# Performance work log

Measured on AMD Instinct MI355X. Metric: run time of the kernel, lower is better.

The kernel has to match this reference:

```python
import jax, jax.numpy as jnp
import numpy as np

D, W, H = 128, 128, 128          # volume obj_shape (d, w, h)
RES_D, RES_H = 180, 180          # detector resolution
SR_D, SR_W, SR_H = 1, 1, 1       # sample rates
BATCH = 4                        # hardcoded batch_size in the torch module


def _trilinear_zeros(vol, cx, cy, cz):
    """torch.grid_sample 5D, mode=trilinear, align_corners=True, padding=zeros.
    vol: [D, W, H]. cx indexes last dim (H), cy indexes W, cz indexes D; all in [-1,1].
    """
    d, w, h = vol.shape
    ix = (cx + 1.0) * 0.5 * (h - 1)
    iy = (cy + 1.0) * 0.5 * (w - 1)
    iz = (cz + 1.0) * 0.5 * (d - 1)
    x0 = jnp.floor(ix); y0 = jnp.floor(iy); z0 = jnp.floor(iz)
    wx1 = ix - x0; wy1 = iy - y0; wz1 = iz - z0
    wx0 = 1.0 - wx1; wy0 = 1.0 - wy1; wz0 = 1.0 - wz1

    def corner(zf, yf, xf, wgt):
        valid = (zf >= 0) & (zf <= d - 1) & (yf >= 0) & (yf <= w - 1) & (xf >= 0) & (xf <= h - 1)
        zi = jnp.clip(zf, 0, d - 1).astype(jnp.int32)
        yi = jnp.clip(yf, 0, w - 1).astype(jnp.int32)
        xi = jnp.clip(xf, 0, h - 1).astype(jnp.int32)
        return jnp.where(valid, vol[zi, yi, xi] * wgt, 0.0)

    return (corner(z0,     y0,     x0,     wz0 * wy0 * wx0)
          + corner(z0,     y0,     x0 + 1, wz0 * wy0 * wx1)
          + corner(z0,     y0 + 1, x0,     wz0 * wy1 * wx0)
          + corner(z0,     y0 + 1, x0 + 1, wz0 * wy1 * wx1)
          + corner(z0 + 1, y0,     x0,     wz1 * wy0 * wx0)
          + corner(z0 + 1, y0,     x0 + 1, wz1 * wy0 * wx1)
          + corner(z0 + 1, y0 + 1, x0,     wz1 * wy1 * wx0)
          + corner(z0 + 1, y0 + 1, x0 + 1, wz1 * wy1 * wx1))


def _project_one(vol, emi_pos, spacing):
    # vol: [D, W, H], emi_pos: [3], spacing: [3]
    K = SR_W * W
    p0y = jnp.linspace(0.0, W - 1.0, K)                     # (P0 - I0)·N, N = [0,1,0]
    lin_x = jnp.linspace(-RES_D / 2.0, RES_D / 2.0 - 1.0, RES_D * SR_D)
    lin_y = jnp.linspace(-RES_H / 2.0, RES_H / 2.0 - 1.0, RES_H * SR_H)
    gx, gy = jnp.meshgrid(lin_x, lin_y, indexing='ij')      # [Nx, Ny]
    I = jnp.stack([gx, jnp.zeros_like(gx), gy], axis=-1) - emi_pos   # [Nx,Ny,3]
    dxv = I / I[..., 1:2]
    dx = jnp.linalg.norm(dxv * spacing, axis=-1)            # per-ray path length [Nx,Ny]
    In = I / jnp.linalg.norm(I, axis=-1, keepdims=True)     # unit ray dirs
    T = (p0y - emi_pos[1])[None, None, :] / In[..., 1:2]    # [Nx,Ny,K]
    grid = In[..., None, :] * T[..., None] + emi_pos        # world points [Nx,Ny,K,3]
    # normalization as in torch code, then torch.flip(grid,[3]) swaps coord order
    cx = grid[..., 2] / H * 2.0          # -> indexes last vol dim (H)
    cy = grid[..., 1] / W * 2.0 - 1.0    # -> indexes W
    cz = grid[..., 0] / D * 2.0          # -> indexes D
    samp = _trilinear_zeros(vol, cx, cy, cz)                # [Nx,Ny,K]
    return jnp.sum(samp, axis=-1) * dx                      # [Nx,Ny]


def setup_inputs() -> dict:
    key = jax.random.key(0)
    k1, k2 = jax.random.split(key)
    I_rec = jax.random.uniform(k1, (1, 1, D, W, H), dtype=jnp.float32)
    # emitters near [0, -300, 0]; y must be far from the y=0 detector plane
    poses = jnp.array([0.0, -300.0, 0.0], jnp.float32) + 5.0 * jax.random.normal(k2, (BATCH, 3), jnp.float32)
    spacing = jnp.ones((3,), jnp.float32)
    return {"I_rec": I_rec, "poses": poses, "spacing": spacing}


def reference(I_rec, poses, spacing):
    vol = I_rec[0, 0]  # [D, W, H]
    # deterministic idx = [0..BATCH-1] (original uses random.sample)
    proj = jax.vmap(_project_one, in_axes=(None, 0, None))(vol, poses[:BATCH], spacing)
    return proj[:, None, :, :]  # [BATCH, 1, RES_D*SR_D, RES_H*SR_H]
```

## Files before the change

### kernel.cpp

```cpp
#include <hip/hip_runtime.h>


#define RES 180
#define NPIX (4 * RES * RES)
#define PIX_PER_BLOCK 32
#define NCHUNK (NPIX / PIX_PER_BLOCK)
#define CHUNK_STRIDE 1013

typedef struct __attribute__((packed, aligned(4))) { float x, y; } f2u;

__global__ __launch_bounds__(256) void proj_kernel(
    const float* __restrict__ vol, const float* __restrict__ poses,
    const float* __restrict__ spacing, float* __restrict__ out) {
  const int tid = threadIdx.x;
  const int lp  = tid & 31;
  const int ks  = tid >> 5;
  const int chunk = (int)(((long long)blockIdx.x * CHUNK_STRIDE) % NCHUNK);
  const int gpix = chunk * PIX_PER_BLOCK + lp;

  const int b   = gpix / (RES * RES);
  const int rem = gpix - b * (RES * RES);
  const int i   = rem / RES;
  const int j   = rem - i * RES;

  const float ex = poses[b * 3 + 0];
  const float ey = poses[b * 3 + 1];
  const float ez = poses[b * 3 + 2];

  const float gx = (float)i - 90.0f;
  const float gy = (float)j - 90.0f;
  const float Ix = gx - ex;
  const float Iy = -ey;
  const float Iz = gy - ez;

  const float c     = 63.5f / 64.0f;
  const float invIy = 1.0f / Iy;

  const float izb = fmaf(ex + Ix, c, 63.5f);
  const float izs = Ix * invIy * c;
  const float ixb = fmaf(ez + Iz, c, 63.5f);
  const float ixs = Iz * invIy * c;

  const int k0 = ks * 16;
  float ka = (float)k0;
  float kb = (float)(k0 + 16);
  {
    if (ixs > 1e-12f)       { ka = fmaxf(ka, (-1.0f - ixb) / ixs); kb = fminf(kb, (128.0f - ixb) / ixs); }
    else if (ixs < -1e-12f) { ka = fmaxf(ka, (128.0f - ixb) / ixs); kb = fminf(kb, (-1.0f - ixb) / ixs); }
    else if (ixb <= -1.0f || ixb >= 128.0f) { kb = ka; }
    if (izs > 1e-12f)       { ka = fmaxf(ka, (-1.0f - izb) / izs); kb = fminf(kb, (128.0f - izb) / izs); }
    else if (izs < -1e-12f) { ka = fmaxf(ka, (128.0f - izb) / izs); kb = fminf(kb, (-1.0f - izb) / izs); }
    else if (izb <= -1.0f || izb >= 128.0f) { kb = ka; }
    ka = fmaxf(ka, (float)k0);
    kb = fminf(kb, (float)(k0 + 16));
  }
  const int kai = (int)ceilf(ka);
  const int kbi = (int)ceilf(kb);

  float sum = 0.0f;
#pragma unroll 2
  for (int k = kai; k < kbi; ++k) {
    const float kf = (float)k;
    const float ix = fmaf(kf, ixs, ixb);
    const float iy = kf * c;
    const float iz = fmaf(kf, izs, izb);

    const float fx = floorf(ix), fy = floorf(iy), fz = floorf(iz);
    const int x0 = (int)fx, y0 = (int)fy, z0 = (int)fz;

    const float wx1 = ix - fx, wy1 = iy - fy, wz1 = iz - fz;
    const float wx0 = 1.0f - wx1, wy0 = 1.0f - wy1, wz0 = 1.0f - wz1;

    const float vx0 = ((unsigned)x0       < 128u) ? wx0 : 0.0f;
    const float vx1 = ((unsigned)(x0 + 1) < 128u) ? wx1 : 0.0f;
    const float vz0 = ((unsigned)z0       < 128u) ? wz0 : 0.0f;
    const float vz1 = ((unsigned)(z0 + 1) < 128u) ? wz1 : 0.0f;

    const int xb2 = min(max(x0, 0), 126);
    const bool in = (x0 == xb2);
    const float wlo = in ? vx0 : vx1;
    const float whi = in ? vx1 : vx0;

    const int zc0 = min(max(z0, 0), 127), zc1 = min(max(z0 + 1, 0), 127);
    const float* base = vol + ((zc0 << 14) + (y0 << 7) + xb2);
    const int dz = (zc1 - zc0) << 14;

    const f2u v00 = *(const f2u*)(base);
    const f2u v01 = *(const f2u*)(base + 128);
    const f2u v10 = *(const f2u*)(base + dz);
    const f2u v11 = *(const f2u*)(base + dz + 128);

    const float s00 = fmaf(whi, v00.y, wlo * v00.x);
    const float s01 = fmaf(whi, v01.y, wlo * v01.x);
    const float s10 = fmaf(whi, v10.y, wlo * v10.x);
    const float s11 = fmaf(whi, v11.y, wlo * v11.x);
    const float s0  = fmaf(wy1, s01, wy0 * s00);
    const float s1  = fmaf(wy1, s11, wy0 * s10);

    sum = fmaf(vz0, s0, sum);
    sum = fmaf(vz1, s1, sum);
  }

  __shared__ float part[256];
  part[tid] = sum;
  __syncthreads();

  if (tid < PIX_PER_BLOCK) {
    float tot = 0.0f;
#pragma unroll
    for (int s = 0; s < 8; ++s) tot += part[tid + 32 * s];
    const float sxp = spacing[0], syp = spacing[1], szp = spacing[2];
    const float ax = Ix * invIy * sxp;
    const float az = Iz * invIy * szp;
    const float dxl = sqrtf(fmaf(ax, ax, fmaf(az, az, syp * syp)));
    out[gpix] = tot * dxl;
  }
}

extern "C" void kernel_launch(void* const* d_in, const int* in_sizes, int n_in,
                              void* d_out, int out_size, void* d_ws, size_t ws_size,
                              hipStream_t stream) {
  const float* vol     = (const float*)d_in[0];
  const float* poses   = (const float*)d_in[1];
  const float* spacing = (const float*)d_in[2];
  float* out = (float*)d_out;

  proj_kernel<<<NCHUNK, 256, 0, stream>>>(vol, poses, spacing, out);
}
```

Baseline: 26.99 us.

## Split ray march into unmasked interior loop and masked edge loops; widen blocks

```diff
diff --git a/kernel.cpp b/kernel.cpp
--- a/kernel.cpp
+++ b/kernel.cpp
@@ -2,26 +2,25 @@
 
 
 #define RES 180
-#define NPIX (4 * RES * RES)
-#define PIX_PER_BLOCK 32
-#define NCHUNK (NPIX / PIX_PER_BLOCK)
+#define JSTRIPS 3
+#define NCHUNK (4 * RES * JSTRIPS)
 #define CHUNK_STRIDE 1013
 
 typedef struct __attribute__((packed, aligned(4))) { float x, y; } f2u;
 
-__global__ __launch_bounds__(256) void proj_kernel(
+__global__ __launch_bounds__(512) void proj_kernel(
     const float* __restrict__ vol, const float* __restrict__ poses,
     const float* __restrict__ spacing, float* __restrict__ out) {
-  const int tid = threadIdx.x;
-  const int lp  = tid & 31;
-  const int ks  = tid >> 5;
+  const int tid  = threadIdx.x;
+  const int lane = tid & 63;
+  const int ks   = tid >> 6;
   const int chunk = (int)(((long long)blockIdx.x * CHUNK_STRIDE) % NCHUNK);
-  const int gpix = chunk * PIX_PER_BLOCK + lp;
-
-  const int b   = gpix / (RES * RES);
-  const int rem = gpix - b * (RES * RES);
-  const int i   = rem / RES;
-  const int j   = rem - i * RES;
+  const int js = chunk % JSTRIPS;
+  const int t  = chunk / JSTRIPS;
+  const int i  = t % RES;
+  const int b  = t / RES;
+  const int j  = js * 64 + lane;
+  const bool live = (j < RES);
 
   const float ex = poses[b * 3 + 0];
   const float ey = poses[b * 3 + 1];
@@ -42,78 +41,114 @@
   const float ixs = Iz * invIy * c;
 
   const int k0 = ks * 16;
-  float ka = (float)k0;
-  float kb = (float)(k0 + 16);
-  {
-    if (ixs > 1e-12f)       { ka = fmaxf(ka, (-1.0f - ixb) / ixs); kb = fminf(kb, (128.0f - ixb) / ixs); }
-    else if (ixs < -1e-12f) { ka = fmaxf(ka, (128.0f - ixb) / ixs); kb = fminf(kb, (-1.0f - ixb) / ixs); }
-    else if (ixb <= -1.0f || ixb >= 128.0f) { kb = ka; }
-    if (izs > 1e-12f)       { ka = fmaxf(ka, (-1.0f - izb) / izs); kb = fminf(kb, (128.0f - izb) / izs); }
-    else if (izs < -1e-12f) { ka = fmaxf(ka, (128.0f - izb) / izs); kb = fminf(kb, (-1.0f - izb) / izs); }
-    else if (izb <= -1.0f || izb >= 128.0f) { kb = ka; }
-    ka = fmaxf(ka, (float)k0);
-    kb = fminf(kb, (float)(k0 + 16));
-  }
+  float ka = (float)k0, kb = (float)(k0 + 16);
+  if (ixs > 1e-12f)       { ka = fmaxf(ka, (-1.0f - ixb) / ixs); kb = fminf(kb, (128.0f - ixb) / ixs); }
+  else if (ixs < -1e-12f) { ka = fmaxf(ka, (128.0f - ixb) / ixs); kb = fminf(kb, (-1.0f - ixb) / ixs); }
+  else if (ixb <= -1.0f || ixb >= 128.0f) { kb = ka; }
+  if (izs > 1e-12f)       { ka = fmaxf(ka, (-1.0f - izb) / izs); kb = fminf(kb, (128.0f - izb) / izs); }
+  else if (izs < -1e-12f) { ka = fmaxf(ka, (128.0f - izb) / izs); kb = fminf(kb, (-1.0f - izb) / izs); }
+  else if (izb <= -1.0f || izb >= 128.0f) { kb = ka; }
+  ka = fmaxf(ka, (float)k0);
+  kb = fminf(kb, (float)(k0 + 16));
   const int kai = (int)ceilf(ka);
-  const int kbi = (int)ceilf(kb);
+  int kbi = (int)ceilf(kb);
+  if (!live) kbi = kai;
+
+  float ia = ka, ib = kb;
+  if (ixs > 1e-12f)       { ia = fmaxf(ia, (1.0f - ixb) / ixs); ib = fminf(ib, (126.0f - ixb) / ixs); }
+  else if (ixs < -1e-12f) { ia = fmaxf(ia, (126.0f - ixb) / ixs); ib = fminf(ib, (1.0f - ixb) / ixs); }
+  else if (ixb < 1.0f || ixb >= 126.0f) { ib = ia; }
+  if (izs > 1e-12f)       { ia = fmaxf(ia, (1.0f - izb) / izs); ib = fminf(ib, (126.0f - izb) / izs); }
+  else if (izs < -1e-12f) { ia = fmaxf(ia, (126.0f - izb) / izs); ib = fminf(ib, (1.0f - izb) / izs); }
+  else if (izb < 1.0f || izb >= 126.0f) { ib = ia; }
+  int m0 = (int)ceilf(fmaxf(ia, 1.0f));
+  int m1 = (int)ceilf(ib);
+  m0 = min(max(m0, kai), kbi);
+  m1 = min(max(m1, m0), kbi);
 
   float sum = 0.0f;
+
+#define MASKED_BODY(k)                                                         \
+  {                                                                            \
+    const float kf = (float)(k);                                               \
+    const float ix = fmaf(kf, ixs, ixb);                                       \
+    const float iy = kf * c;                                                   \
+    const float iz = fmaf(kf, izs, izb);                                       \
+    const float fx = floorf(ix), fy = floorf(iy), fz = floorf(iz);             \
+    const int x0 = (int)fx, y0 = (int)fy, z0 = (int)fz;                        \
+    const float wx1 = ix - fx, wy1 = iy - fy, wz1 = iz - fz;                   \
+    const float wx0 = 1.0f - wx1, wy0 = 1.0f - wy1, wz0 = 1.0f - wz1;          \
+    const float vx0 = ((unsigned)x0       < 128u) ? wx0 : 0.0f;                \
+    const float vx1 = ((unsigned)(x0 + 1) < 128u) ? wx1 : 0.0f;                \
+    const float vz0 = ((unsigned)z0       < 128u) ? wz0 : 0.0f;                \
+    const float vz1 = ((unsigned)(z0 + 1) < 128u) ? wz1 : 0.0f;                \
+    const int xb2 = min(max(x0, 0), 126);                                      \
+    const bool in = (x0 == xb2);                                               \
+    const float wlo = in ? vx0 : vx1;                                          \
+    const float whi = in ? vx1 : vx0;                                          \
+    const int zc0 = min(max(z0, 0), 127), zc1 = min(max(z0 + 1, 0), 127);      \
+    const float* base = vol + ((zc0 << 14) + (y0 << 7) + xb2);                 \
+    const int dz = (zc1 - zc0) << 14;                                          \
+    const f2u v00 = *(const f2u*)(base);                                       \
+    const f2u v01 = *(const f2u*)(base + 128);                                 \
+    const f2u v10 = *(const f2u*)(base + dz);                                  \
+    const f2u v11 = *(const f2u*)(base + dz + 128);                            \
+    const float s00 = fmaf(whi, v00.y, wlo * v00.x);                           \
+    const float s01 = fmaf(whi, v01.y, wlo * v01.x);                           \
+    const float s10 = fmaf(whi, v10.y, wlo * v10.x);                           \
+    const float s11 = fmaf(whi, v11.y, wlo * v11.x);                           \
+    const float s0  = fmaf(wy1, s01, wy0 * s00);                               \
+    const float s1  = fmaf(wy1, s11, wy0 * s10);                               \
+    sum = fmaf(vz0, s0, sum);                                                  \
+    sum = fmaf(vz1, s1, sum);                                                  \
+  }
+
+  for (int k = kai; k < m0; ++k) MASKED_BODY(k)
+
 #pragma unroll 2
-  for (int k = kai; k < kbi; ++k) {
+  for (int k = m0; k < m1; ++k) {
     const float kf = (float)k;
     const float ix = fmaf(kf, ixs, ixb);
-    const float iy = kf * c;
     const float iz = fmaf(kf, izs, izb);
+    const float fx = floorf(ix), fz = floorf(iz);
+    const int x0 = (int)fx, z0 = (int)fz;
+    const float wx1 = ix - fx, wz1 = iz - fz;
+    const float wx0 = 1.0f - wx1, wz0 = 1.0f - wz1;
+    const float wy0 = kf * 0.0078125f;
+    const float wy1 = 1.0f - wy0;
 
-    const float fx = floorf(ix), fy = floorf(iy), fz = floorf(iz);
-    const int x0 = (int)fx, y0 = (int)fy, z0 = (int)fz;
+    const float* p = vol + ((z0 << 14) + (k << 7) - 128 + x0);
+    const f2u v00 = *(const f2u*)(p);
+    const f2u v01 = *(const f2u*)(p + 128);
+    const f2u v10 = *(const f2u*)(p + 16384);
+    const f2u v11 = *(const f2u*)(p + 16384 + 128);
 
-    const float wx1 = ix - fx, wy1 = iy - fy, wz1 = iz - fz;
-    const float wx0 = 1.0f - wx1, wy0 = 1.0f - wy1, wz0 = 1.0f - wz1;
-
-    const float vx0 = ((unsigned)x0       < 128u) ? wx0 : 0.0f;
-    const float vx1 = ((unsigned)(x0 + 1) < 128u) ? wx1 : 0.0f;
-    const float vz0 = ((unsigned)z0       < 128u) ? wz0 : 0.0f;
-    const float vz1 = ((unsigned)(z0 + 1) < 128u) ? wz1 : 0.0f;
-
-    const int xb2 = min(max(x0, 0), 126);
-    const bool in = (x0 == xb2);
-    const float wlo = in ? vx0 : vx1;
-    const float whi = in ? vx1 : vx0;
-
-    const int zc0 = min(max(z0, 0), 127), zc1 = min(max(z0 + 1, 0), 127);
-    const float* base = vol + ((zc0 << 14) + (y0 << 7) + xb2);
-    const int dz = (zc1 - zc0) << 14;
-
-    const f2u v00 = *(const f2u*)(base);
-    const f2u v01 = *(const f2u*)(base + 128);
-    const f2u v10 = *(const f2u*)(base + dz);
-    const f2u v11 = *(const f2u*)(base + dz + 128);
-
-    const float s00 = fmaf(whi, v00.y, wlo * v00.x);
-    const float s01 = fmaf(whi, v01.y, wlo * v01.x);
-    const float s10 = fmaf(whi, v10.y, wlo * v10.x);
-    const float s11 = fmaf(whi, v11.y, wlo * v11.x);
+    const float s00 = fmaf(wx1, v00.y, wx0 * v00.x);
+    const float s01 = fmaf(wx1, v01.y, wx0 * v01.x);
+    const float s10 = fmaf(wx1, v10.y, wx0 * v10.x);
+    const float s11 = fmaf(wx1, v11.y, wx0 * v11.x);
     const float s0  = fmaf(wy1, s01, wy0 * s00);
     const float s1  = fmaf(wy1, s11, wy0 * s10);
-
-    sum = fmaf(vz0, s0, sum);
-    sum = fmaf(vz1, s1, sum);
+    sum = fmaf(wz0, s0, sum);
+    sum = fmaf(wz1, s1, sum);
   }
 
-  __shared__ float part[256];
+  for (int k = m1; k < kbi; ++k) MASKED_BODY(k)
+#undef MASKED_BODY
+
+  __shared__ float part[512];
   part[tid] = sum;
   __syncthreads();
 
-  if (tid < PIX_PER_BLOCK) {
+  if (tid < 64 && live) {
     float tot = 0.0f;
 #pragma unroll
-    for (int s = 0; s < 8; ++s) tot += part[tid + 32 * s];
+    for (int s = 0; s < 8; ++s) tot += part[tid + 64 * s];
     const float sxp = spacing[0], syp = spacing[1], szp = spacing[2];
     const float ax = Ix * invIy * sxp;
     const float az = Iz * invIy * szp;
     const float dxl = sqrtf(fmaf(ax, ax, fmaf(az, az, syp * syp)));
-    out[gpix] = tot * dxl;
+    out[((b * RES) + i) * RES + j] = tot * dxl;
   }
 }
 
@@ -125,5 +160,5 @@
   const float* spacing = (const float*)d_in[2];
   float* out = (float*)d_out;
 
-  proj_kernel<<<NCHUNK, 256, 0, stream>>>(vol, poses, spacing, out);
+  proj_kernel<<<NCHUNK, 512, 0, stream>>>(vol, poses, spacing, out);
 }
```

Result: slower. 46.16 us (+71.0%).

## Pre-pad volume with zero borders and remap rays into 64-wide row strips

Applied to the files above, without the earlier changes.

```diff
diff --git a/kernel.cpp b/kernel.cpp
--- a/kernel.cpp
+++ b/kernel.cpp
@@ -2,61 +2,159 @@
 
 
 #define RES 180
-#define NPIX (4 * RES * RES)
-#define PIX_PER_BLOCK 32
-#define NCHUNK (NPIX / PIX_PER_BLOCK)
+#define JSTRIPS 3
+#define NCHUNK (4 * RES * JSTRIPS)
 #define CHUNK_STRIDE 1013
 
+#define PH 130
+#define PW 128
+#define PD 130
+#define PSLAB (PW * PH)
+#define PAD_ELEMS (PD * PSLAB)
+#define PAD_FRONT ((size_t)(PSLAB + PH + 128) * 4)
+#define PAD_TAIL  ((size_t)(PSLAB + PH + 128) * 4)
+#define WS_NEED (PAD_FRONT + (size_t)PAD_ELEMS * 4 + PAD_TAIL)
+#define PAD_OFF_EL (PSLAB + 1)
+
 typedef struct __attribute__((packed, aligned(4))) { float x, y; } f2u;
 
-__global__ __launch_bounds__(256) void proj_kernel(
+__global__ __launch_bounds__(256) void pad_kernel(
+    const float* __restrict__ vol, float* __restrict__ pad) {
+  const int t = blockIdx.x * 256 + threadIdx.x;
+  const int z = blockIdx.y;
+  if (t >= PSLAB) return;
+  const int y = t / PH;
+  const int x = t - y * PH;
+  float v = 0.0f;
+  if (z >= 1 && z <= 128 && x >= 1 && x <= 128)
+    v = vol[(((z - 1)) << 14) + (y << 7) + (x - 1)];
+  pad[z * PSLAB + t] = v;
+}
+
+__global__ __launch_bounds__(512) void proj_pad_kernel(
+    const float* __restrict__ pad, const float* __restrict__ poses,
+    const float* __restrict__ spacing, float* __restrict__ out) {
+  const int tid  = threadIdx.x;
+  const int lane = tid & 63;
+  const int ks   = tid >> 6;
+  const int chunk = (int)(((long long)blockIdx.x * CHUNK_STRIDE) % NCHUNK);
+  const int js = chunk % JSTRIPS;
+  const int t  = chunk / JSTRIPS;
+  const int i  = t % RES;
+  const int b  = t / RES;
+  const int j  = js * 64 + lane;
+  const bool live = (j < RES);
+
+  const float ex = poses[b * 3 + 0];
+  const float ey = poses[b * 3 + 1];
+  const float ez = poses[b * 3 + 2];
+
+  const float gx = (float)i - 90.0f;
+  const float gy = (float)j - 90.0f;
+  const float Ix = gx - ex;
+  const float Iy = -ey;
+  const float Iz = gy - ez;
+
+  const float c     = 63.5f / 64.0f;
+  const float invIy = 1.0f / Iy;
+
+  const float izb = fmaf(ex + Ix, c, 63.5f);
+  const float izs = Ix * invIy * c;
+  const float ixb = fmaf(ez + Iz, c, 63.5f);
+  const float ixs = Iz * invIy * c;
+
+  const int k0 = ks * 16;
+  float ka = (float)k0, kb = (float)(k0 + 16);
+  if (ixs > 1e-12f)       { ka = fmaxf(ka, (-1.0f - ixb) / ixs); kb = fminf(kb, (128.0f - ixb) / ixs); }
+  else if (ixs < -1e-12f) { ka = fmaxf(ka, (128.0f - ixb) / ixs); kb = fminf(kb, (-1.0f - ixb) / ixs); }
+  else if (ixb <= -1.0f || ixb >= 128.0f) { kb = ka; }
+  if (izs > 1e-12f)       { ka = fmaxf(ka, (-1.0f - izb) / izs); kb = fminf(kb, (128.0f - izb) / izs); }
+  else if (izs < -1e-12f) { ka = fmaxf(ka, (128.0f - izb) / izs); kb = fminf(kb, (-1.0f - izb) / izs); }
+  else if (izb <= -1.0f || izb >= 128.0f) { kb = ka; }
+  ka = fmaxf(ka, (float)k0);
+  kb = fminf(kb, (float)(k0 + 16));
+  const int kai = (int)ceilf(ka);
+  int kbi = (int)ceilf(kb);
+  if (!live) kbi = kai;
+
+  const float* pbase = pad + PAD_OFF_EL;
+
+  float sum = 0.0f;
+#pragma unroll 2
+  for (int k = kai; k < kbi; ++k) {
+    const float kf = (float)k;
+    const float ix = fmaf(kf, ixs, ixb);
+    const float iz = fmaf(kf, izs, izb);
+    const float fx = floorf(ix), fz = floorf(iz);
+    const int x0 = (int)fx, z0 = (int)fz;
+    const float wx1 = ix - fx, wz1 = iz - fz;
+    const float wx0 = 1.0f - wx1, wz0 = 1.0f - wz1;
+    const float wyA = kf * 0.0078125f;
+    const float wyB = 1.0f - wyA;
+
+    const float* p = pbase + (z0 * PSLAB + (k - 1) * PH + x0);
+    const f2u v00 = *(const f2u*)(p);
+    const f2u v01 = *(const f2u*)(p + PH);
+    const f2u v10 = *(const f2u*)(p + PSLAB);
+    const f2u v11 = *(const f2u*)(p + PSLAB + PH);
+
+    const float s00 = fmaf(wx1, v00.y, wx0 * v00.x);
+    const float s01 = fmaf(wx1, v01.y, wx0 * v01.x);
+    const float s10 = fmaf(wx1, v10.y, wx0 * v10.x);
+    const float s11 = fmaf(wx1, v11.y, wx0 * v11.x);
+    const float s0  = fmaf(wyB, s01, wyA * s00);
+    const float s1  = fmaf(wyB, s11, wyA * s10);
+    sum = fmaf(wz0, s0, sum);
+    sum = fmaf(wz1, s1, sum);
+  }
+
+  __shared__ float part[512];
+  part[tid] = sum;
+  __syncthreads();
+
+  if (tid < 64 && live) {
+    float tot = 0.0f;
+#pragma unroll
+    for (int s = 0; s < 8; ++s) tot += part[tid + 64 * s];
+    const float sxp = spacing[0], syp = spacing[1], szp = spacing[2];
+    const float ax = Ix * invIy * sxp;
+    const float az = Iz * invIy * szp;
+    const float dxl = sqrtf(fmaf(ax, ax, fmaf(az, az, syp * syp)));
+    out[((b * RES) + i) * RES + j] = tot * dxl;
+  }
+}
+
+#define F_PPB 32
+#define F_NCHUNK (4 * RES * RES / F_PPB)
+__global__ __launch_bounds__(256) void proj_masked_kernel(
     const float* __restrict__ vol, const float* __restrict__ poses,
     const float* __restrict__ spacing, float* __restrict__ out) {
   const int tid = threadIdx.x;
   const int lp  = tid & 31;
   const int ks  = tid >> 5;
-  const int chunk = (int)(((long long)blockIdx.x * CHUNK_STRIDE) % NCHUNK);
-  const int gpix = chunk * PIX_PER_BLOCK + lp;
-
+  const int chunk = (int)(((long long)blockIdx.x * 1013) % F_NCHUNK);
+  const int gpix = chunk * F_PPB + lp;
   const int b   = gpix / (RES * RES);
   const int rem = gpix - b * (RES * RES);
   const int i   = rem / RES;
   const int j   = rem - i * RES;
-
-  const float ex = poses[b * 3 + 0];
-  const float ey = poses[b * 3 + 1];
-  const float ez = poses[b * 3 + 2];
-
-  const float gx = (float)i - 90.0f;
-  const float gy = (float)j - 90.0f;
-  const float Ix = gx - ex;
-  const float Iy = -ey;
-  const float Iz = gy - ez;
-
-  const float c     = 63.5f / 64.0f;
-  const float invIy = 1.0f / Iy;
-
-  const float izb = fmaf(ex + Ix, c, 63.5f);
-  const float izs = Ix * invIy * c;
-  const float ixb = fmaf(ez + Iz, c, 63.5f);
-  const float ixs = Iz * invIy * c;
-
+  const float ex = poses[b * 3 + 0], ey = poses[b * 3 + 1], ez = poses[b * 3 + 2];
+  const float gx = (float)i - 90.0f, gy = (float)j - 90.0f;
+  const float Ix = gx - ex, Iy = -ey, Iz = gy - ez;
+  const float c = 63.5f / 64.0f, invIy = 1.0f / Iy;
+  const float izb = fmaf(ex + Ix, c, 63.5f), izs = Ix * invIy * c;
+  const float ixb = fmaf(ez + Iz, c, 63.5f), ixs = Iz * invIy * c;
   const int k0 = ks * 16;
-  float ka = (float)k0;
-  float kb = (float)(k0 + 16);
-  {
-    if (ixs > 1e-12f)       { ka = fmaxf(ka, (-1.0f - ixb) / ixs); kb = fminf(kb, (128.0f - ixb) / ixs); }
-    else if (ixs < -1e-12f) { ka = fmaxf(ka, (128.0f - ixb) / ixs); kb = fminf(kb, (-1.0f - ixb) / ixs); }
-    else if (ixb <= -1.0f || ixb >= 128.0f) { kb = ka; }
-    if (izs > 1e-12f)       { ka = fmaxf(ka, (-1.0f - izb) / izs); kb = fminf(kb, (128.0f - izb) / izs); }
-    else if (izs < -1e-12f) { ka = fmaxf(ka, (128.0f - izb) / izs); kb = fminf(kb, (-1.0f - izb) / izs); }
-    else if (izb <= -1.0f || izb >= 128.0f) { kb = ka; }
-    ka = fmaxf(ka, (float)k0);
-    kb = fminf(kb, (float)(k0 + 16));
-  }
+  float ka = (float)k0, kb = (float)(k0 + 16);
+  if (ixs > 1e-12f)       { ka = fmaxf(ka, (-1.0f - ixb) / ixs); kb = fminf(kb, (128.0f - ixb) / ixs); }
+  else if (ixs < -1e-12f) { ka = fmaxf(ka, (128.0f - ixb) / ixs); kb = fminf(kb, (-1.0f - ixb) / ixs); }
+  else if (ixb <= -1.0f || ixb >= 128.0f) { kb = ka; }
+  if (izs > 1e-12f)       { ka = fmaxf(ka, (-1.0f - izb) / izs); kb = fminf(kb, (128.0f - izb) / izs); }
+  else if (izs < -1e-12f) { ka = fmaxf(ka, (128.0f - izb) / izs); kb = fminf(kb, (-1.0f - izb) / izs); }
+  else if (izb <= -1.0f || izb >= 128.0f) { kb = ka; }
+  ka = fmaxf(ka, (float)k0); kb = fminf(kb, (float)(k0 + 16));
   const int kai = (int)ceilf(ka);
   const int kbi = (int)ceilf(kb);
-
   float sum = 0.0f;
 #pragma unroll 2
   for (int k = kai; k < kbi; ++k) {
@@ -64,48 +162,38 @@
     const float ix = fmaf(kf, ixs, ixb);
     const float iy = kf * c;
     const float iz = fmaf(kf, izs, izb);
-
     const float fx = floorf(ix), fy = floorf(iy), fz = floorf(iz);
     const int x0 = (int)fx, y0 = (int)fy, z0 = (int)fz;
-
     const float wx1 = ix - fx, wy1 = iy - fy, wz1 = iz - fz;
     const float wx0 = 1.0f - wx1, wy0 = 1.0f - wy1, wz0 = 1.0f - wz1;
-
     const float vx0 = ((unsigned)x0       < 128u) ? wx0 : 0.0f;
     const float vx1 = ((unsigned)(x0 + 1) < 128u) ? wx1 : 0.0f;
     const float vz0 = ((unsigned)z0       < 128u) ? wz0 : 0.0f;
     const float vz1 = ((unsigned)(z0 + 1) < 128u) ? wz1 : 0.0f;
-
     const int xb2 = min(max(x0, 0), 126);
     const bool in = (x0 == xb2);
     const float wlo = in ? vx0 : vx1;
     const float whi = in ? vx1 : vx0;
-
     const int zc0 = min(max(z0, 0), 127), zc1 = min(max(z0 + 1, 0), 127);
     const float* base = vol + ((zc0 << 14) + (y0 << 7) + xb2);
     const int dz = (zc1 - zc0) << 14;
-
     const f2u v00 = *(const f2u*)(base);
     const f2u v01 = *(const f2u*)(base + 128);
     const f2u v10 = *(const f2u*)(base + dz);
     const f2u v11 = *(const f2u*)(base + dz + 128);
-
     const float s00 = fmaf(whi, v00.y, wlo * v00.x);
     const float s01 = fmaf(whi, v01.y, wlo * v01.x);
     const float s10 = fmaf(whi, v10.y, wlo * v10.x);
     const float s11 = fmaf(whi, v11.y, wlo * v11.x);
     const float s0  = fmaf(wy1, s01, wy0 * s00);
     const float s1  = fmaf(wy1, s11, wy0 * s10);
-
     sum = fmaf(vz0, s0, sum);
     sum = fmaf(vz1, s1, sum);
   }
-
   __shared__ float part[256];
   part[tid] = sum;
   __syncthreads();
-
-  if (tid < PIX_PER_BLOCK) {
+  if (tid < F_PPB) {
     float tot = 0.0f;
 #pragma unroll
     for (int s = 0; s < 8; ++s) tot += part[tid + 32 * s];
@@ -125,5 +213,12 @@
   const float* spacing = (const float*)d_in[2];
   float* out = (float*)d_out;
 
-  proj_kernel<<<NCHUNK, 256, 0, stream>>>(vol, poses, spacing, out);
-}
+  if (ws_size >= WS_NEED) {
+    float* pad = (float*)((char*)d_ws + PAD_FRONT);
+    dim3 pg((PSLAB + 255) / 256, PD);
+    pad_kernel<<<pg, 256, 0, stream>>>(vol, pad);
+    proj_pad_kernel<<<NCHUNK, 512, 0, stream>>>(pad, poses, spacing, out);
+  } else {
+    proj_masked_kernel<<<F_NCHUNK * 2, 256, 0, stream>>>(vol, poses, spacing, out);
+  }
+}
```

Result: slower. 41.05 us (+52.1%).

## Split projection into per-segment partial kernel plus reduction with unmasked interior loop

Applied to the files above, without the earlier changes.

```diff
diff --git a/kernel.cpp b/kernel.cpp
--- a/kernel.cpp
+++ b/kernel.cpp
@@ -3,60 +3,216 @@
 
 #define RES 180
 #define NPIX (4 * RES * RES)
-#define PIX_PER_BLOCK 32
-#define NCHUNK (NPIX / PIX_PER_BLOCK)
-#define CHUNK_STRIDE 1013
+#define PB_N 507
+#define PB_STRIDE 251
+#define NG 8
+#define BIG (1 << 29)
 
 typedef struct __attribute__((packed, aligned(4))) { float x, y; } f2u;
 
-__global__ __launch_bounds__(256) void proj_kernel(
+__global__ __launch_bounds__(256) void proj_part_kernel(
+    const float* __restrict__ vol, const float* __restrict__ poses,
+    float* __restrict__ part) {
+  const int g  = blockIdx.x & 7;
+  const int pb = (int)(((blockIdx.x >> 3) * PB_STRIDE) % PB_N);
+  const int gpix = pb * 256 + threadIdx.x;
+  const bool live = (gpix < NPIX);
+  const int gp  = live ? gpix : (NPIX - 1);
+
+  const int b   = gp / (RES * RES);
+  const int rem = gp - b * (RES * RES);
+  const int i   = rem / RES;
+  const int j   = rem - i * RES;
+
+  const float ex = poses[b * 3 + 0];
+  const float ey = poses[b * 3 + 1];
+  const float ez = poses[b * 3 + 2];
+
+  const float Ix = ((float)i - 90.0f) - ex;
+  const float Iy = -ey;
+  const float Iz = ((float)j - 90.0f) - ez;
+
+  const float c     = 63.5f / 64.0f;
+  const float invIy = 1.0f / Iy;
+
+  const float izb = fmaf(ex + Ix, c, 63.5f);
+  const float izs = Ix * invIy * c;
+  const float ixb = fmaf(ez + Iz, c, 63.5f);
+  const float ixs = Iz * invIy * c;
+
+  const int k0 = g * 16;
+  float ka = (float)k0, kb = (float)(k0 + 16);
+  if (ixs > 1e-12f)       { ka = fmaxf(ka, (-1.0f - ixb) / ixs); kb = fminf(kb, (128.0f - ixb) / ixs); }
+  else if (ixs < -1e-12f) { ka = fmaxf(ka, (128.0f - ixb) / ixs); kb = fminf(kb, (-1.0f - ixb) / ixs); }
+  else if (ixb <= -1.0f || ixb >= 128.0f) { kb = ka; }
+  if (izs > 1e-12f)       { ka = fmaxf(ka, (-1.0f - izb) / izs); kb = fminf(kb, (128.0f - izb) / izs); }
+  else if (izs < -1e-12f) { ka = fmaxf(ka, (128.0f - izb) / izs); kb = fminf(kb, (-1.0f - izb) / izs); }
+  else if (izb <= -1.0f || izb >= 128.0f) { kb = ka; }
+  ka = fmaxf(ka, (float)k0);
+  kb = fminf(kb, (float)(k0 + 16));
+  int kai = (int)ceilf(ka);
+  int kbi = (int)ceilf(kb);
+  if (!live) kbi = kai;
+  const bool valid = (kbi > kai);
+
+  float ia = ka, ib = kb;
+  if (ixs > 1e-12f)       { ia = fmaxf(ia, (1.0f - ixb) / ixs); ib = fminf(ib, (126.0f - ixb) / ixs); }
+  else if (ixs < -1e-12f) { ia = fmaxf(ia, (126.0f - ixb) / ixs); ib = fminf(ib, (1.0f - ixb) / ixs); }
+  else if (ixb < 1.0f || ixb >= 126.0f) { ib = ia; }
+  if (izs > 1e-12f)       { ia = fmaxf(ia, (1.0f - izb) / izs); ib = fminf(ib, (126.0f - izb) / izs); }
+  else if (izs < -1e-12f) { ia = fmaxf(ia, (126.0f - izb) / izs); ib = fminf(ib, (1.0f - izb) / izs); }
+  else if (izb < 1.0f || izb >= 126.0f) { ib = ia; }
+  int m0 = min(max((int)ceilf(ia), kai), kbi);
+  int m1 = min(max((int)ceilf(ib), m0), kbi);
+  const bool hasInt = valid && (m1 > m0);
+
+  int kaiw = valid ? kai : BIG;
+  int kbiw = valid ? kbi : -BIG;
+  int m0w  = hasInt ? m0 : BIG;
+  int m1w  = hasInt ? m1 : BIG;
+#pragma unroll
+  for (int m = 32; m >= 1; m >>= 1) {
+    kaiw = min(kaiw, __shfl_xor(kaiw, m));
+    kbiw = max(kbiw, __shfl_xor(kbiw, m));
+    m0w  = max(m0w,  __shfl_xor(m0w,  m));
+    m1w  = min(m1w,  __shfl_xor(m1w,  m));
+  }
+  m0w = min(max(m0w, kaiw), kbiw);
+  m1w = min(max(m1w, m0w), kbiw);
+
+  float sum = 0.0f;
+
+#define MASKED_BODY(k)                                                         \
+  if (k >= kai && k < kbi) {                                                   \
+    const float kf = (float)(k);                                               \
+    const float ix = fmaf(kf, ixs, ixb);                                       \
+    const float iz = fmaf(kf, izs, izb);                                       \
+    const float fx = floorf(ix), fz = floorf(iz);                              \
+    const int x0 = (int)fx, z0 = (int)fz;                                      \
+    const float wx1 = ix - fx, wz1 = iz - fz;                                  \
+    const float wx0 = 1.0f - wx1, wz0 = 1.0f - wz1;                            \
+    const float wyA = kf * 0.0078125f;           \
+    const float wyB = 1.0f - wyA;                  \
+    const int yoffA = max((k) - 1, 0) << 7;                                    \
+    const int yoffB = (k) << 7;                                                \
+    const float vx0 = ((unsigned)x0       < 128u) ? wx0 : 0.0f;                \
+    const float vx1 = ((unsigned)(x0 + 1) < 128u) ? wx1 : 0.0f;                \
+    const float vz0 = ((unsigned)z0       < 128u) ? wz0 : 0.0f;                \
+    const float vz1 = ((unsigned)(z0 + 1) < 128u) ? wz1 : 0.0f;                \
+    const int xb2 = min(max(x0, 0), 126);                                      \
+    const bool inx = (x0 == xb2);                                              \
+    const float wlo = inx ? vx0 : vx1;                                         \
+    const float whi = inx ? vx1 : vx0;                                         \
+    const int zc0 = min(max(z0, 0), 127), zc1 = min(max(z0 + 1, 0), 127);      \
+    const float* base = vol + ((zc0 << 14) + xb2);                             \
+    const int dz = (zc1 - zc0) << 14;                                          \
+    const f2u v00 = *(const f2u*)(base + yoffA);                               \
+    const f2u v01 = *(const f2u*)(base + yoffB);                               \
+    const f2u v10 = *(const f2u*)(base + dz + yoffA);                          \
+    const f2u v11 = *(const f2u*)(base + dz + yoffB);                          \
+    const float s00 = fmaf(whi, v00.y, wlo * v00.x);                           \
+    const float s01 = fmaf(whi, v01.y, wlo * v01.x);                           \
+    const float s10 = fmaf(whi, v10.y, wlo * v10.x);                           \
+    const float s11 = fmaf(whi, v11.y, wlo * v11.x);                           \
+    const float s0  = fmaf(wyB, s01, wyA * s00);                               \
+    const float s1  = fmaf(wyB, s11, wyA * s10);                               \
+    sum = fmaf(vz0, s0, sum);                                                  \
+    sum = fmaf(vz1, s1, sum);                                                  \
+  }
+
+  for (int k = kaiw; k < m0w; ++k) MASKED_BODY(k)
+
+#pragma unroll 2
+  for (int k = m0w; k < m1w; ++k) {
+    const float kf = (float)k;
+    const float ix = fmaf(kf, ixs, ixb);
+    const float iz = fmaf(kf, izs, izb);
+    const float fx = floorf(ix), fz = floorf(iz);
+    const int x0 = (int)fx, z0 = (int)fz;
+    const float wx1 = ix - fx, wz1 = iz - fz;
+    const float wx0 = 1.0f - wx1, wz0 = 1.0f - wz1;
+    const float wyA = kf * 0.0078125f;
+    const float wyB = 1.0f - wyA;
+    const int yoffA = max(k - 1, 0) << 7;
+    const int yoffB = k << 7;
+
+    const float* p0 = vol + ((z0 << 14) + x0);
+    const f2u v00 = *(const f2u*)(p0 + yoffA);
+    const f2u v01 = *(const f2u*)(p0 + yoffB);
+    const f2u v10 = *(const f2u*)(p0 + 16384 + yoffA);
+    const f2u v11 = *(const f2u*)(p0 + 16384 + yoffB);
+
+    const float s00 = fmaf(wx1, v00.y, wx0 * v00.x);
+    const float s01 = fmaf(wx1, v01.y, wx0 * v01.x);
+    const float s10 = fmaf(wx1, v10.y, wx0 * v10.x);
+    const float s11 = fmaf(wx1, v11.y, wx0 * v11.x);
+    const float s0  = fmaf(wyB, s01, wyA * s00);
+    const float s1  = fmaf(wyB, s11, wyA * s10);
+    sum = fmaf(wz0, s0, sum);
+    sum = fmaf(wz1, s1, sum);
+  }
+
+  for (int k = m1w; k < kbiw; ++k) MASKED_BODY(k)
+#undef MASKED_BODY
+
+  if (live) part[g * NPIX + gpix] = sum;
+}
+
+__global__ __launch_bounds__(256) void reduce_kernel(
+    const float* __restrict__ part, const float* __restrict__ poses,
+    const float* __restrict__ spacing, float* __restrict__ out) {
+  const int p = blockIdx.x * 256 + threadIdx.x;
+  if (p >= NPIX) return;
+  float s = 0.0f;
+#pragma unroll
+  for (int g = 0; g < NG; ++g) s += part[g * NPIX + p];
+
+  const int b   = p / (RES * RES);
+  const int rem = p - b * (RES * RES);
+  const int i   = rem / RES;
+  const int j   = rem - i * RES;
+  const float ex = poses[b * 3 + 0];
+  const float ey = poses[b * 3 + 1];
+  const float ez = poses[b * 3 + 2];
+  const float Ix = ((float)i - 90.0f) - ex;
+  const float Iz = ((float)j - 90.0f) - ez;
+  const float invIy = 1.0f / (-ey);
+  const float ax = Ix * invIy * spacing[0];
+  const float az = Iz * invIy * spacing[2];
+  const float sy = spacing[1];
+  out[p] = s * sqrtf(fmaf(ax, ax, fmaf(az, az, sy * sy)));
+}
+
+#define F_PPB 32
+#define F_NCHUNK (NPIX / F_PPB)
+__global__ __launch_bounds__(256) void proj_masked_kernel(
     const float* __restrict__ vol, const float* __restrict__ poses,
     const float* __restrict__ spacing, float* __restrict__ out) {
   const int tid = threadIdx.x;
   const int lp  = tid & 31;
   const int ks  = tid >> 5;
-  const int chunk = (int)(((long long)blockIdx.x * CHUNK_STRIDE) % NCHUNK);
-  const int gpix = chunk * PIX_PER_BLOCK + lp;
-
+  const int chunk = (int)(((long long)blockIdx.x * 1013) % F_NCHUNK);
+  const int gpix = chunk * F_PPB + lp;
   const int b   = gpix / (RES * RES);
   const int rem = gpix - b * (RES * RES);
   const int i   = rem / RES;
   const int j   = rem - i * RES;
-
-  const float ex = poses[b * 3 + 0];
-  const float ey = poses[b * 3 + 1];
-  const float ez = poses[b * 3 + 2];
-
-  const float gx = (float)i - 90.0f;
-  const float gy = (float)j - 90.0f;
-  const float Ix = gx - ex;
-  const float Iy = -ey;
-  const float Iz = gy - ez;
-
-  const float c     = 63.5f / 64.0f;
-  const float invIy = 1.0f / Iy;
-
-  const float izb = fmaf(ex + Ix, c, 63.5f);
-  const float izs = Ix * invIy * c;
-  const float ixb = fmaf(ez + Iz, c, 63.5f);
-  const float ixs = Iz * invIy * c;
-
+  const float ex = poses[b * 3 + 0], ey = poses[b * 3 + 1], ez = poses[b * 3 + 2];
+  const float Ix = ((float)i - 90.0f) - ex, Iy = -ey, Iz = ((float)j - 90.0f) - ez;
+  const float c = 63.5f / 64.0f, invIy = 1.0f / Iy;
+  const float izb = fmaf(ex + Ix, c, 63.5f), izs = Ix * invIy * c;
+  const float ixb = fmaf(ez + Iz, c, 63.5f), ixs = Iz * invIy * c;
   const int k0 = ks * 16;
-  float ka = (float)k0;
-  float kb = (float)(k0 + 16);
-  {
-    if (ixs > 1e-12f)       { ka = fmaxf(ka, (-1.0f - ixb) / ixs); kb = fminf(kb, (128.0f - ixb) / ixs); }
-    else if (ixs < -1e-12f) { ka = fmaxf(ka, (128.0f - ixb) / ixs); kb = fminf(kb, (-1.0f - ixb) / ixs); }
-    else if (ixb <= -1.0f || ixb >= 128.0f) { kb = ka; }
-    if (izs > 1e-12f)       { ka = fmaxf(ka, (-1.0f - izb) / izs); kb = fminf(kb, (128.0f - izb) / izs); }
-    else if (izs < -1e-12f) { ka = fmaxf(ka, (128.0f - izb) / izs); kb = fminf(kb, (-1.0f - izb) / izs); }
-    else if (izb <= -1.0f || izb >= 128.0f) { kb = ka; }
-    ka = fmaxf(ka, (float)k0);
-    kb = fminf(kb, (float)(k0 + 16));
-  }
+  float ka = (float)k0, kb = (float)(k0 + 16);
+  if (ixs > 1e-12f)       { ka = fmaxf(ka, (-1.0f - ixb) / ixs); kb = fminf(kb, (128.0f - ixb) / ixs); }
+  else if (ixs < -1e-12f) { ka = fmaxf(ka, (128.0f - ixb) / ixs); kb = fminf(kb, (-1.0f - ixb) / ixs); }
+  else if (ixb <= -1.0f || ixb >= 128.0f) { kb = ka; }
+  if (izs > 1e-12f)       { ka = fmaxf(ka, (-1.0f - izb) / izs); kb = fminf(kb, (128.0f - izb) / izs); }
+  else if (izs < -1e-12f) { ka = fmaxf(ka, (128.0f - izb) / izs); kb = fminf(kb, (-1.0f - izb) / izs); }
+  else if (izb <= -1.0f || izb >= 128.0f) { kb = ka; }
+  ka = fmaxf(ka, (float)k0); kb = fminf(kb, (float)(k0 + 16));
   const int kai = (int)ceilf(ka);
   const int kbi = (int)ceilf(kb);
-
   float sum = 0.0f;
 #pragma unroll 2
   for (int k = kai; k < kbi; ++k) {
@@ -64,56 +220,45 @@
     const float ix = fmaf(kf, ixs, ixb);
     const float iy = kf * c;
     const float iz = fmaf(kf, izs, izb);
-
     const float fx = floorf(ix), fy = floorf(iy), fz = floorf(iz);
     const int x0 = (int)fx, y0 = (int)fy, z0 = (int)fz;
-
     const float wx1 = ix - fx, wy1 = iy - fy, wz1 = iz - fz;
     const float wx0 = 1.0f - wx1, wy0 = 1.0f - wy1, wz0 = 1.0f - wz1;
-
     const float vx0 = ((unsigned)x0       < 128u) ? wx0 : 0.0f;
     const float vx1 = ((unsigned)(x0 + 1) < 128u) ? wx1 : 0.0f;
     const float vz0 = ((unsigned)z0       < 128u) ? wz0 : 0.0f;
     const float vz1 = ((unsigned)(z0 + 1) < 128u) ? wz1 : 0.0f;
-
     const int xb2 = min(max(x0, 0), 126);
-    const bool in = (x0 == xb2);
-    const float wlo = in ? vx0 : vx1;
-    const float whi = in ? vx1 : vx0;
-
+    const bool inx = (x0 == xb2);
+    const float wlo = inx ? vx0 : vx1;
+    const float whi = inx ? vx1 : vx0;
     const int zc0 = min(max(z0, 0), 127), zc1 = min(max(z0 + 1, 0), 127);
     const float* base = vol + ((zc0 << 14) + (y0 << 7) + xb2);
     const int dz = (zc1 - zc0) << 14;
-
     const f2u v00 = *(const f2u*)(base);
     const f2u v01 = *(const f2u*)(base + 128);
     const f2u v10 = *(const f2u*)(base + dz);
     const f2u v11 = *(const f2u*)(base + dz + 128);
-
     const float s00 = fmaf(whi, v00.y, wlo * v00.x);
     const float s01 = fmaf(whi, v01.y, wlo * v01.x);
     const float s10 = fmaf(whi, v10.y, wlo * v10.x);
     const float s11 = fmaf(whi, v11.y, wlo * v11.x);
     const float s0  = fmaf(wy1, s01, wy0 * s00);
     const float s1  = fmaf(wy1, s11, wy0 * s10);
-
     sum = fmaf(vz0, s0, sum);
     sum = fmaf(vz1, s1, sum);
   }
-
   __shared__ float part[256];
   part[tid] = sum;
   __syncthreads();
-
-  if (tid < PIX_PER_BLOCK) {
+  if (tid < F_PPB) {
     float tot = 0.0f;
 #pragma unroll
     for (int s = 0; s < 8; ++s) tot += part[tid + 32 * s];
-    const float sxp = spacing[0], syp = spacing[1], szp = spacing[2];
-    const float ax = Ix * invIy * sxp;
-    const float az = Iz * invIy * szp;
-    const float dxl = sqrtf(fmaf(ax, ax, fmaf(az, az, syp * syp)));
-    out[gpix] = tot * dxl;
+    const float ax = Ix * invIy * spacing[0];
+    const float az = Iz * invIy * spacing[2];
+    const float sy = spacing[1];
+    out[gpix] = tot * sqrtf(fmaf(ax, ax, fmaf(az, az, sy * sy)));
   }
 }
 
@@ -125,5 +270,12 @@
   const float* spacing = (const float*)d_in[2];
   float* out = (float*)d_out;
 
-  proj_kernel<<<NCHUNK, 256, 0, stream>>>(vol, poses, spacing, out);
-}
+  const size_t need = (size_t)NG * NPIX * sizeof(float);
+  if (ws_size >= need) {
+    float* part = (float*)d_ws;
+    proj_part_kernel<<<NG * PB_N, 256, 0, stream>>>(vol, poses, part);
+    reduce_kernel<<<PB_N, 256, 0, stream>>>(part, poses, spacing, out);
+  } else {
+    proj_masked_kernel<<<F_NCHUNK, 256, 0, stream>>>(vol, poses, spacing, out);
+  }
+}
```

Result: slower. 34.55 us (+28.0%).
